# Kernel tuning notes

Hardware: AMD Instinct MI355X
Metric: run time of the kernel (lower is better)

## Reference

```python
import jax, jax.numpy as jnp
import numpy as np

B, T, N, C = 32, 12, 1024, 2   # batch, lookback window, n_series, in_channels
D, H, K, OUT = 16, 64, 2, 12   # embedding_dim, rnn_units, cheb_k, out_dim (horizon)


def setup_inputs() -> dict:
    key = jax.random.key(0)
    ks = jax.random.split(key, 12)
    p = lambda k, sh, s=0.1: jax.random.normal(k, sh, dtype=jnp.float32) * s
    return {
        "source": jax.random.normal(ks[0], (B, T, N, C), dtype=jnp.float32),
        "node_emb": p(ks[1], (N, D), 0.3),
        # layer 0: dim_in = C + H
        "gate_w0": p(ks[2], (D, K, C + H, 2 * H)),
        "gate_b0": p(ks[3], (D, 2 * H)),
        "upd_w0": p(ks[4], (D, K, C + H, H)),
        "upd_b0": p(ks[5], (D, H)),
        # layer 1: dim_in = H + H
        "gate_w1": p(ks[6], (D, K, 2 * H, 2 * H)),
        "gate_b1": p(ks[7], (D, 2 * H)),
        "upd_w1": p(ks[8], (D, K, 2 * H, H)),
        "upd_b1": p(ks[9], (D, H)),
        # end_conv: Conv2d(1, OUT*out_channels, kernel=(1,H)) == linear over hidden dim
        "conv_w": p(ks[10], (OUT, H)),
        "conv_b": p(ks[11], (OUT,)),
    }


def _supports(node_emb):
    # softmax(relu(E E^T)) row-normalized adaptive adjacency; Chebyshev stack (K, N, N)
    A = jax.nn.softmax(jax.nn.relu(node_emb @ node_emb.T), axis=1)
    s = [jnp.eye(N, dtype=A.dtype), A]
    for _ in range(2, K):
        s.append(2.0 * A @ s[-1] - s[-2])
    return jnp.stack(s, axis=0)


def _gcn(x, node_emb, w_pool, b_pool, supports):
    # x: (B, N, Cin); per-node adaptive weights from pools
    w = jnp.einsum('nd,dkio->nkio', node_emb, w_pool)     # (N, K, Cin, Cout)
    b = node_emb @ b_pool                                 # (N, Cout)
    xg = jnp.einsum('knm,bmc->bnkc', supports, x)         # (B, N, K, Cin)
    return jnp.einsum('bnki,nkio->bno', xg, w) + b


def _layer(x_seq, node_emb, supports, gw, gb, uw, ub):
    # x_seq: (B, T, N, Cin) -> (B, T, N, H) via GRU-style AGCRN cell, scanned over T
    def step(state, x_t):
        inp = jnp.concatenate([x_t, state], axis=-1)
        zr = jax.nn.sigmoid(_gcn(inp, node_emb, gw, gb, supports))
        z, r = jnp.split(zr, 2, axis=-1)
        cand = jnp.concatenate([x_t, z * state], axis=-1)
        hc = jnp.tanh(_gcn(cand, node_emb, uw, ub, supports))
        h = r * state + (1.0 - r) * hc
        return h, h

    init = jnp.zeros((x_seq.shape[0], N, H), dtype=x_seq.dtype)
    _, hs = jax.lax.scan(step, init, jnp.swapaxes(x_seq, 0, 1))
    return jnp.swapaxes(hs, 0, 1)


def reference(source, node_emb, gate_w0, gate_b0, upd_w0, upd_b0,
              gate_w1, gate_b1, upd_w1, upd_b1, conv_w, conv_b,
              teacher_forcing_ratio=0):
    sup = _supports(node_emb)  # adaptive supports depend only on static node_emb
    h1 = _layer(source, node_emb, sup, gate_w0, gate_b0, upd_w0, upd_b0)
    h2 = _layer(h1, node_emb, sup, gate_w1, gate_b1, upd_w1, upd_b1)
    last = h2[:, -1]  # (B, N, H)
    # end_conv over hidden dim -> (B, OUT, N); out_channels==1 so squeeze folds away
    out = jnp.einsum('bnh,oh->bon', last, conv_w) + conv_b[None, :, None]
    return out
```

## Files before the change

### kernel.cpp

```cpp
#include <hip/hip_runtime.h>
#include <hip/hip_fp16.h>


typedef _Float16 f16x8 __attribute__((ext_vector_type(8)));
typedef _Float16 f16x4 __attribute__((ext_vector_type(4)));
typedef float f32x4 __attribute__((ext_vector_type(4)));

#define WAIT_VM0 asm volatile("s_waitcnt vmcnt(0)" ::: "memory")
#define WAIT_VM1 asm volatile("s_waitcnt vmcnt(1)" ::: "memory")
#define WAIT_VM2 asm volatile("s_waitcnt vmcnt(2)" ::: "memory")
#define WAIT_VM1_LG asm volatile("s_waitcnt vmcnt(1) lgkmcnt(0)" ::: "memory")
#define WAIT_VM2_LG asm volatile("s_waitcnt vmcnt(2) lgkmcnt(0)" ::: "memory")
#define WAIT_LG asm volatile("s_waitcnt lgkmcnt(0)" ::: "memory")
#define BARRIER do { __builtin_amdgcn_s_barrier(); asm volatile("" ::: "memory"); } while (0)

__device__ __forceinline__ void gload_lds16(const void* g, void* l) {
  __builtin_amdgcn_global_load_lds(
      (const __attribute__((address_space(1))) void*)g,
      (__attribute__((address_space(3))) void*)l, 16, 0, 0);
}

__device__ __forceinline__ void dma_g128(const _Float16* Wc, _Float16* buf, int tid) {
  int wave = tid >> 6;
#pragma unroll
  for (int u = 0; u < 2; ++u) {
    gload_lds16(Wc + (size_t)(u * 256 + tid) * 8,
                buf + (size_t)(u * 256 + wave * 64) * 8);
  }
}

__device__ __forceinline__ void dma_g64(const _Float16* Wc, _Float16* buf, int tid) {
  int wave = tid >> 6;
  gload_lds16(Wc + (size_t)tid * 8, buf + (size_t)(wave * 64) * 8);
}

__device__ __forceinline__ f16x8 wrd(const _Float16* buf, int o, int s) {
  int flat = (o & 7) | (((s ^ (o & 3)) & 3) << 3) | ((o >> 3) << 5);
  return *(const f16x8*)(buf + flat * 8);
}

__global__ __launch_bounds__(256) void compute_A_kernel(const float* __restrict__ E,
                                                        __half* __restrict__ Ah) {
  int n = blockIdx.x;
  int tid = threadIdx.x;
  __shared__ float red[256];
  float en[16];
#pragma unroll
  for (int d = 0; d < 16; ++d) en[d] = E[n * 16 + d];
  float v[4];
#pragma unroll
  for (int q = 0; q < 4; ++q) {
    int m = tid + q * 256;
    const float* Em = E + m * 16;
    float dot = 0.f;
#pragma unroll
    for (int d = 0; d < 16; ++d) dot += en[d] * Em[d];
    v[q] = fmaxf(dot, 0.f);
  }
  float mx = fmaxf(fmaxf(v[0], v[1]), fmaxf(v[2], v[3]));
  red[tid] = mx; __syncthreads();
  for (int s = 128; s > 0; s >>= 1) { if (tid < s) red[tid] = fmaxf(red[tid], red[tid + s]); __syncthreads(); }
  mx = red[0];
  __syncthreads();
  float e[4], sum = 0.f;
#pragma unroll
  for (int q = 0; q < 4; ++q) { e[q] = expf(v[q] - mx); sum += e[q]; }
  red[tid] = sum; __syncthreads();
  for (int s = 128; s > 0; s >>= 1) { if (tid < s) red[tid] += red[tid + s]; __syncthreads(); }
  float inv = 1.f / red[0];
#pragma unroll
  for (int q = 0; q < 4; ++q) Ah[(size_t)n * 1024 + tid + q * 256] = __float2half(e[q] * inv);
}

__global__ __launch_bounds__(256) void pool_t16_kernel(const float* __restrict__ gw0,
                                                       const float* __restrict__ uw0,
                                                       const float* __restrict__ gw1,
                                                       const float* __restrict__ uw1,
                                                       __half* __restrict__ poolT16) {
  int rg = blockIdx.x;
  const float* pool; int F, O, TK; size_t jb; int kk, jj, i;
  if (rg < 128)      { pool = gw0; F = 66;  O = 128; TK = 64;  jb = 0;     kk = rg >> 6; jj = rg & 63; i = jj + 2; }
  else if (rg < 256) { int r = rg - 128; pool = uw0; F = 66;  O = 64;  TK = 64;  jb = 16384; kk = r >> 6; jj = r & 63;  i = jj + 2; }
  else if (rg < 512) { int r = rg - 256; pool = gw1; F = 128; O = 128; TK = 128; jb = 24576; kk = r >> 7; jj = r & 127; i = jj; }
  else               { int r = rg - 512; pool = uw1; F = 128; O = 64;  TK = 128; jb = 57344; kk = r >> 7; jj = r & 127; i = jj; }
  int o = threadIdx.x;
  if (o >= O) return;
  f16x8 a, b, zz = {};
#pragma unroll
  for (int d = 0; d < 8; ++d)
    a[d] = (_Float16)pool[(((size_t)d * 2 + kk) * F + i) * O + o];
#pragma unroll
  for (int d = 8; d < 16; ++d)
    b[d - 8] = (_Float16)pool[(((size_t)d * 2 + kk) * F + i) * O + o];
  size_t j = jb + (size_t)o * (2 * TK) + (size_t)kk * TK + jj;
  _Float16* outp = (_Float16*)poolT16 + j * 32;
  *(f16x8*)outp = a;
  *(f16x8*)(outp + 8) = b;
  *(f16x8*)(outp + 16) = zz;
  *(f16x8*)(outp + 24) = zz;
}

__global__ __launch_bounds__(256) void prelude_misc_kernel(
    const float* __restrict__ E, __half* __restrict__ E16,
    const float* __restrict__ gb0, const float* __restrict__ ub0,
    const float* __restrict__ gb1, const float* __restrict__ ub1,
    float* __restrict__ Bg0, float* __restrict__ Bu0,
    float* __restrict__ Bg1, float* __restrict__ Bu1,
    const float* __restrict__ src, __half* __restrict__ x16,
    const float* __restrict__ gw0, const float* __restrict__ uw0,
    float* __restrict__ WxG0, float* __restrict__ WxU0,
    float4* __restrict__ zero_p) {
  int bid = blockIdx.x;
  if (bid < 8192) {
    int i = bid * 256 + threadIdx.x;
    zero_p[i] = float4{0.f, 0.f, 0.f, 0.f};
    return;
  }
  bid -= 8192;
  if (bid < 384) {
    int t0 = bid >> 5, b = bid & 31;
    const float* s = src + (size_t)(b * 12 + t0) * 2048;
    __half* dst = x16 + t0 * 64 + b * 2;
    for (int nn = threadIdx.x; nn < 1024; nn += 256) {
      float2 v = *(const float2*)(s + nn * 2);
      *(__half2*)(dst + (size_t)nn * 768) = __floats2half2_rn(v.x, v.y);
    }
    return;
  }
  bid -= 384;
  if (bid < 1536) {
    int tid = bid * 256 + threadIdx.x;
    if (tid >= 1024 * 384) return;
    int n = tid / 384, c = tid - n * 384;
    const float* pool; float* outp; int O, o;
    if (c < 128)      { pool = gb0; outp = Bg0; O = 128; o = c; }
    else if (c < 192) { pool = ub0; outp = Bu0; O = 64;  o = c - 128; }
    else if (c < 320) { pool = gb1; outp = Bg1; O = 128; o = c - 192; }
    else              { pool = ub1; outp = Bu1; O = 64;  o = c - 320; }
    const float* En = E + n * 16;
    float a = 0.f;
#pragma unroll
    for (int d = 0; d < 16; ++d) a += En[d] * pool[d * O + o];
    outp[n * O + o] = a;
    return;
  }
  bid -= 1536;
  if (bid < 128) {
    int t = bid * 256 + threadIdx.x;
    int d = t & 31;
    E16[t] = (d < 16) ? __float2half(E[(t >> 5) * 16 + d]) : __half(0);
    return;
  }
  bid -= 128;
  if (bid < 2048) {
    int v = bid * 256 + threadIdx.x;
    int n = v >> 9, q = (v >> 7) & 3, o = v & 127;
    int kk = q >> 1, c = q & 1;
    const float* En = E + n * 16;
    float a = 0.f;
#pragma unroll
    for (int d = 0; d < 16; ++d)
      a += En[d] * gw0[(((size_t)d * 2 + kk) * 66 + c) * 128 + o];
    WxG0[(size_t)n * 512 + q * 128 + o] = __half2float(__float2half(a));
    return;
  }
  bid -= 2048;
  {
    int v = bid * 256 + threadIdx.x;
    int n = v >> 8, q = (v >> 6) & 3, o = v & 63;
    int kk = q >> 1, c = q & 1;
    const float* En = E + n * 16;
    float a = 0.f;
#pragma unroll
    for (int d = 0; d < 16; ++d)
      a += En[d] * uw0[(((size_t)d * 2 + kk) * 66 + c) * 64 + o];
    WxU0[(size_t)n * 256 + q * 64 + o] = __half2float(__float2half(a));
  }
}

__global__ __launch_bounds__(256) void make_wt_mfma_kernel(
    const __half* __restrict__ E16g, const __half* __restrict__ poolT16g,
    __half* __restrict__ WtG0, __half* __restrict__ WtU0,
    __half* __restrict__ WtG1, __half* __restrict__ WtU1) {
  __shared__ __align__(16) _Float16 Es[64][40];
  __shared__ __align__(16) _Float16 wbuf[64][264];
  const _Float16* E16 = (const _Float16*)E16g;
  const _Float16* pT = (const _Float16*)poolT16g;
  int bx = blockIdx.x;
  __half* Wt; int O, KIP, segbase, kc, og;
  if (bx < 64)       { Wt = WtG0; O = 128; KIP = 128; segbase = 0;     kc = bx & 3;  og = bx >> 2; }
  else if (bx < 96)  { int b = bx - 64;  Wt = WtU0; O = 64;  KIP = 128; segbase = 16384; kc = b & 3; og = b >> 2; }
  else if (bx < 224) { int b = bx - 96;  Wt = WtG1; O = 128; KIP = 256; segbase = 24576; kc = b & 7; og = b >> 3; }
  else               { int b = bx - 224; Wt = WtU1; O = 64;  KIP = 256; segbase = 57344; kc = b & 7; og = b >> 3; }
  int o0 = og * 8;
  int n0 = blockIdx.y * 64;
  {
    int r = threadIdx.x >> 2, ch = (threadIdx.x & 3) * 8;
    *(f16x8*)&Es[r][ch] = *(const f16x8*)(E16 + (size_t)(n0 + r) * 32 + ch);
  }
  __syncthreads();
  int wave = threadIdx.x >> 6, lane = threadIdx.x & 63;
  int fm = lane & 15, fg = lane >> 4;
  f16x8 af[4];
#pragma unroll
  for (int i = 0; i < 4; ++i) af[i] = *(const f16x8*)&Es[i * 16 + fm][fg * 8];
  f32x4 acc[4][4] = {};
#pragma unroll
  for (int jt = 0; jt < 4; ++jt) {
    int local = wave * 64 + jt * 16 + fm;
    int oo = local >> 5, kip = local & 31;
    size_t jc = (size_t)segbase + (size_t)(o0 + oo) * KIP + kc * 32 + kip;
    f16x8 bf = *(const f16x8*)(pT + jc * 32 + fg * 8);
#pragma unroll
    for (int i = 0; i < 4; ++i)
      acc[i][jt] = __builtin_amdgcn_mfma_f32_16x16x32_f16(af[i], bf, acc[i][jt], 0, 0, 0);
  }
#pragma unroll
  for (int i = 0; i < 4; ++i)
#pragma unroll
    for (int jt = 0; jt < 4; ++jt)
#pragma unroll
      for (int r = 0; r < 4; ++r)
        wbuf[i * 16 + fg * 4 + r][wave * 64 + jt * 16 + fm] = (_Float16)acc[i][jt][r];
  __syncthreads();
  int NCH = KIP >> 5;
  int CH = O * 32;
  int sbase = (o0 >> 3) * 256;
  for (int idx = threadIdx.x; idx < 64 * 32; idx += 256) {
    int nsub = idx >> 5, w = idx & 31;
    int oo = w & 7;
    int s = (w >> 3) ^ (w & 3);
    int pos = oo * 32 + s * 8;
    size_t dst = ((size_t)(n0 + nsub) * NCH + kc) * CH + sbase + (size_t)w * 8;
    *(float4*)(Wt + dst) = *(float4*)&wbuf[nsub][pos];
  }
}

__global__ __launch_bounds__(256) void gemm_nt_kernel(
    const __half* __restrict__ Ahg, const __half* __restrict__ X0g,
    const __half* __restrict__ X1g, __half* __restrict__ Yg,
    int Nc, int cstride, int split) {
  __shared__ __align__(16) _Float16 As[64][136];
  __shared__ __align__(16) _Float16 Bs[64][144];
  const _Float16* __restrict__ Ah = (const _Float16*)Ahg;
  _Float16* __restrict__ Y = (_Float16*)Yg;
  int tid = threadIdx.x;
  int row0 = blockIdx.y * 64;
  int col0 = blockIdx.x * 64;
  const _Float16* __restrict__ Xsrc =
      (col0 < split) ? (const _Float16*)X0g : (const _Float16*)X1g;
  int colg = (col0 < split) ? col0 : col0 - split;
  int wave = tid >> 6, lane = tid & 63;
  int wm = wave & 1, wn = wave >> 1;
  int fm = lane & 15, fg = lane >> 4;

  int sr = tid >> 2, sc = (tid & 3) * 32;
  const _Float16* pa = Ah + (size_t)(row0 + sr) * 1024 + sc;
  int kq = tid & 31, cg = tid >> 5;
  int kb = 4 * kq;
  const _Float16* pb = Xsrc + (size_t)kb * cstride + colg + cg * 8;
  int chunk = kq >> 1;
  int kin = (kq & 1) * 4;

  f16x8 ra[4], rb[4];
#pragma unroll
  for (int c = 0; c < 4; ++c) ra[c] = *(const f16x8*)(pa + c * 8);
#pragma unroll
  for (int r = 0; r < 4; ++r) rb[r] = *(const f16x8*)(pb + (size_t)r * cstride);

  f32x4 acc[2][2] = {};
  for (int k0 = 0; k0 < 1024; k0 += 128) {
#pragma unroll
    for (int c = 0; c < 4; ++c) *(f16x8*)&As[sr][sc + c * 8] = ra[c];
#pragma unroll
    for (int i = 0; i < 8; ++i) {
      int c = cg * 8 + i;
      f16x4 p;
      p[0] = rb[0][i]; p[1] = rb[1][i]; p[2] = rb[2][i]; p[3] = rb[3][i];
      *(f16x4*)&Bs[c][((chunk ^ (c & 7)) << 3) + kin] = p;
    }
    __syncthreads();
    if (k0 + 128 < 1024) {
#pragma unroll
      for (int c = 0; c < 4; ++c) ra[c] = *(const f16x8*)(pa + k0 + 128 + c * 8);
#pragma unroll
      for (int r = 0; r < 4; ++r)
        rb[r] = *(const f16x8*)(pb + (size_t)(k0 + 128 + r) * cstride);
    }
#pragma unroll
    for (int kc = 0; kc < 4; ++kc) {
      int ck = kc * 4 + fg;
      f16x8 af[2], bf[2];
#pragma unroll
      for (int i = 0; i < 2; ++i)
        af[i] = *(const f16x8*)&As[wm * 32 + i * 16 + fm][kc * 32 + fg * 8];
#pragma unroll
      for (int j = 0; j < 2; ++j) {
        int cl = wn * 32 + j * 16 + fm;
        bf[j] = *(const f16x8*)&Bs[cl][(ck ^ (cl & 7)) << 3];
      }
#pragma unroll
      for (int i = 0; i < 2; ++i)
#pragma unroll
        for (int j = 0; j < 2; ++j)
          acc[i][j] = __builtin_amdgcn_mfma_f32_16x16x32_f16(af[i], bf[j], acc[i][j], 0, 0, 0);
    }
    __syncthreads();
  }
#pragma unroll
  for (int i = 0; i < 2; ++i) {
#pragma unroll
    for (int j = 0; j < 2; ++j) {
      int col = col0 + wn * 32 + j * 16 + fm;
      int rbase = row0 + wm * 32 + i * 16 + fg * 4;
#pragma unroll
      for (int r = 0; r < 4; ++r)
        Y[(size_t)(rbase + r) * Nc + col] = (_Float16)acc[i][j][r];
    }
  }
}

__global__ __launch_bounds__(256) void gemm_nt128_kernel(
    const __half* __restrict__ Ahg, const __half* __restrict__ X0g,
    const __half* __restrict__ X1g, __half* __restrict__ Yg,
    int Nc, int cstride, int split) {
  __shared__ __align__(16) _Float16 As[64][136];
  __shared__ __align__(16) _Float16 Bs[128][144];
  const _Float16* __restrict__ Ah = (const _Float16*)Ahg;
  _Float16* __restrict__ Y = (_Float16*)Yg;
  int tid = threadIdx.x;
  int row0 = blockIdx.y * 64;
  int col0 = blockIdx.x * 128;
  const _Float16* __restrict__ Xsrc =
      (col0 < split) ? (const _Float16*)X0g : (const _Float16*)X1g;
  int colg = (col0 < split) ? col0 : col0 - split;
  int wave = tid >> 6, lane = tid & 63;
  int fm = lane & 15, fg = lane >> 4;

  int sr = tid >> 2, sc = (tid & 3) * 32;
  const _Float16* pa = Ah + (size_t)(row0 + sr) * 1024 + sc;
  int kq = tid & 31, cg = tid >> 5;
  int kb = 4 * kq;
  const _Float16* pb = Xsrc + (size_t)kb * cstride + colg + cg * 16;
  int chunk = kq >> 1;
  int kin = (kq & 1) * 4;

  f16x8 ra[4], rb[4][2];
#pragma unroll
  for (int c = 0; c < 4; ++c) ra[c] = *(const f16x8*)(pa + c * 8);
#pragma unroll
  for (int r = 0; r < 4; ++r)
#pragma unroll
    for (int h = 0; h < 2; ++h)
      rb[r][h] = *(const f16x8*)(pb + (size_t)r * cstride + h * 8);

  f32x4 acc[4][2] = {};
  for (int k0 = 0; k0 < 1024; k0 += 128) {
#pragma unroll
    for (int c = 0; c < 4; ++c) *(f16x8*)&As[sr][sc + c * 8] = ra[c];
#pragma unroll
    for (int h = 0; h < 2; ++h)
#pragma unroll
      for (int i = 0; i < 8; ++i) {
        int c = cg * 16 + h * 8 + i;
        f16x4 p;
        p[0] = rb[0][h][i]; p[1] = rb[1][h][i]; p[2] = rb[2][h][i]; p[3] = rb[3][h][i];
        *(f16x4*)&Bs[c][((chunk ^ (c & 7)) << 3) + kin] = p;
      }
    __syncthreads();
    if (k0 + 128 < 1024) {
#pragma unroll
      for (int c = 0; c < 4; ++c) ra[c] = *(const f16x8*)(pa + k0 + 128 + c * 8);
#pragma unroll
      for (int r = 0; r < 4; ++r)
#pragma unroll
        for (int h = 0; h < 2; ++h)
          rb[r][h] = *(const f16x8*)(pb + (size_t)(k0 + 128 + r) * cstride + h * 8);
    }
#pragma unroll
    for (int kc = 0; kc < 4; ++kc) {
      int ck = kc * 4 + fg;
      f16x8 af[4], bf[2];
#pragma unroll
      for (int i = 0; i < 4; ++i)
        af[i] = *(const f16x8*)&As[i * 16 + fm][kc * 32 + fg * 8];
#pragma unroll
      for (int j = 0; j < 2; ++j) {
        int cl = wave * 32 + j * 16 + fm;
        bf[j] = *(const f16x8*)&Bs[cl][(ck ^ (cl & 7)) << 3];
      }
#pragma unroll
      for (int i = 0; i < 4; ++i)
#pragma unroll
        for (int j = 0; j < 2; ++j)
          acc[i][j] = __builtin_amdgcn_mfma_f32_16x16x32_f16(af[i], bf[j], acc[i][j], 0, 0, 0);
    }
    __syncthreads();
  }
#pragma unroll
  for (int i = 0; i < 4; ++i) {
#pragma unroll
    for (int j = 0; j < 2; ++j) {
      int col = col0 + wave * 32 + j * 16 + fm;
      int rbase = row0 + i * 16 + fg * 4;
#pragma unroll
      for (int r = 0; r < 4; ++r)
        Y[(size_t)(rbase + r) * Nc + col] = (_Float16)acc[i][j][r];
    }
  }
}

__device__ __forceinline__ f16x8 ld_g0(const __half* __restrict__ h16,
                                       const __half* __restrict__ YBD, int n, int idx) {
  int b = idx >> 4, part = (idx >> 3) & 1, ch = idx & 7;
  const _Float16* s = part ? (const _Float16*)YBD + (size_t)n * 4096 + b * 64 + ch * 8
                           : (const _Float16*)h16 + (size_t)n * 2048 + b * 64 + ch * 8;
  return *(const f16x8*)s;
}
__device__ __forceinline__ f16x8 ld_u0(const __half* __restrict__ zh0,
                                       const __half* __restrict__ YCE, int n, int idx) {
  int b = idx >> 4, part = (idx >> 3) & 1, ch = idx & 7;
  const _Float16* s = part ? (const _Float16*)YCE + (size_t)n * 4096 + 2048 + b * 64 + ch * 8
                           : (const _Float16*)zh0 + (size_t)n * 2048 + b * 64 + ch * 8;
  return *(const f16x8*)s;
}

__device__ __forceinline__ void gate0_body(
    _Float16* Xs, float (*xq)[4], _Float16 (*Wb)[4096], int n, int t,
    f16x8 pre0, f16x8 pre1, float2 xv, unsigned axu,
    const _Float16* Wn, const float* __restrict__ Bg, const float* __restrict__ Wxg,
    const float* __restrict__ h32, __half* __restrict__ zh0, __half* __restrict__ r0) {
  constexpr int STRIDE = 136;
  {
    int b0 = t >> 4, p0 = (t >> 3) & 1, c0 = t & 7;
    *(f16x8*)&Xs[b0 * STRIDE + p0 * 64 + c0 * 8] = pre0;
    int idx = t + 256;
    int b1 = idx >> 4, p1 = (idx >> 3) & 1, c1 = idx & 7;
    *(f16x8*)&Xs[b1 * STRIDE + p1 * 64 + c1 * 8] = pre1;
  }
  if (t < 32) {
    __half2 ah = *(__half2*)&axu;
    float2 af2 = __half22float2(ah);
    xq[t][0] = __half2float(__float2half(xv.x));
    xq[t][1] = __half2float(__float2half(xv.y));
    xq[t][2] = af2.x; xq[t][3] = af2.y;
  }
  int wave = t >> 6, lane = t & 63;
  int fm = lane & 15, fg = lane >> 4;
  f32x4 acc[2][2] = {};
#pragma unroll
  for (int kc = 0; kc < 4; ++kc) {
    if (kc == 0) WAIT_VM2_LG;
    else if (kc < 3) WAIT_VM2;
    else WAIT_VM0;
    BARRIER;
    const _Float16* wb = Wb[kc & 1];
    f16x8 af[2], bf[2];
#pragma unroll
    for (int i = 0; i < 2; ++i)
      af[i] = *(const f16x8*)&Xs[(i * 16 + fm) * STRIDE + kc * 32 + fg * 8];
#pragma unroll
    for (int j = 0; j < 2; ++j)
      bf[j] = wrd(wb, wave * 32 + j * 16 + fm, fg);
    WAIT_LG;
    BARRIER;
    if (kc < 2) dma_g128(Wn + (size_t)(kc + 2) * 4096, Wb[kc & 1], t);
    __builtin_amdgcn_s_setprio(1);
#pragma unroll
    for (int i = 0; i < 2; ++i)
#pragma unroll
      for (int j = 0; j < 2; ++j)
        acc[i][j] = __builtin_amdgcn_mfma_f32_16x16x32_f16(af[i], bf[j], acc[i][j], 0, 0, 0);
    __builtin_amdgcn_s_setprio(0);
  }
  const float* Bn = Bg + n * 128;
  const float* Wx = Wxg + (size_t)n * 512;
#pragma unroll
  for (int j = 0; j < 2; ++j) {
    int o = wave * 32 + j * 16 + fm;
    float bias = Bn[o];
    float w0 = Wx[o], w1 = Wx[128 + o], w2 = Wx[256 + o], w3 = Wx[384 + o];
#pragma unroll
    for (int i = 0; i < 2; ++i)
#pragma unroll
      for (int r = 0; r < 4; ++r) {
        int b = i * 16 + fg * 4 + r;
        float px = acc[i][j][r] + bias +
                   w0 * xq[b][0] + w1 * xq[b][1] + w2 * xq[b][2] + w3 * xq[b][3];
        float s = 1.f / (1.f + __expf(-px));
        size_t base = (size_t)n * 2048 + b * 64;
        if (o < 64) zh0[base + o] = __float2half(s * h32[base + o]);
        else        r0[base + o - 64] = __float2half(s);
      }
  }
}

__device__ __forceinline__ void upd0_body(
    _Float16* Xs, float (*xq)[4], _Float16 (*Wb)[2048], int n, int t,
    f16x8 pre0, f16x8 pre1, float2 xv, unsigned axu,
    const _Float16* Wn, const float* __restrict__ Bu, const float* __restrict__ Wxu,
    const __half* __restrict__ r0, float* __restrict__ h32, __half* __restrict__ h16) {
  constexpr int STRIDE = 136;
  {
    int b0 = t >> 4, p0 = (t >> 3) & 1, c0 = t & 7;
    *(f16x8*)&Xs[b0 * STRIDE + p0 * 64 + c0 * 8] = pre0;
    int idx = t + 256;
    int b1 = idx >> 4, p1 = (idx >> 3) & 1, c1 = idx & 7;
    *(f16x8*)&Xs[b1 * STRIDE + p1 * 64 + c1 * 8] = pre1;
  }
  if (t < 32) {
    __half2 ah = *(__half2*)&axu;
    float2 af2 = __half22float2(ah);
    xq[t][0] = __half2float(__float2half(xv.x));
    xq[t][1] = __half2float(__float2half(xv.y));
    xq[t][2] = af2.x; xq[t][3] = af2.y;
  }
  int wave = t >> 6, lane = t & 63;
  int fm = lane & 15, fg = lane >> 4;
  f32x4 acc[2] = {};
#pragma unroll
  for (int kc = 0; kc < 4; ++kc) {
    if (kc == 0) WAIT_VM1_LG;
    else if (kc < 3) WAIT_VM1;
    else WAIT_VM0;
    BARRIER;
    const _Float16* wb = Wb[kc & 1];
    f16x8 bf = wrd(wb, wave * 16 + fm, fg);
    f16x8 af0 = *(const f16x8*)&Xs[(0 * 16 + fm) * STRIDE + kc * 32 + fg * 8];
    f16x8 af1 = *(const f16x8*)&Xs[(1 * 16 + fm) * STRIDE + kc * 32 + fg * 8];
    WAIT_LG;
    BARRIER;
    if (kc < 2) dma_g64(Wn + (size_t)(kc + 2) * 2048, Wb[kc & 1], t);
    __builtin_amdgcn_s_setprio(1);
    acc[0] = __builtin_amdgcn_mfma_f32_16x16x32_f16(af0, bf, acc[0], 0, 0, 0);
    acc[1] = __builtin_amdgcn_mfma_f32_16x16x32_f16(af1, bf, acc[1], 0, 0, 0);
    __builtin_amdgcn_s_setprio(0);
  }
  int o = wave * 16 + fm;
  float bias = Bu[n * 64 + o];
  const float* Wx = Wxu + (size_t)n * 256;
  float w0 = Wx[o], w1 = Wx[64 + o], w2 = Wx[128 + o], w3 = Wx[192 + o];
#pragma unroll
  for (int i = 0; i < 2; ++i)
#pragma unroll
    for (int r = 0; r < 4; ++r) {
      int b = i * 16 + fg * 4 + r;
      float x = acc[i][r] + bias +
                w0 * xq[b][0] + w1 * xq[b][1] + w2 * xq[b][2] + w3 * xq[b][3];
      x = fminf(fmaxf(x, -15.f), 15.f);
      float e = __expf(2.f * x);
      float hc = (e - 1.f) / (e + 1.f);
      size_t base = (size_t)n * 2048 + b * 64;
      float rr = __half2float(r0[base + o]);
      float hnew = rr * h32[base + o] + (1.f - rr) * hc;
      h32[base + o] = hnew;
      h16[base + o] = __float2half(hnew);
    }
}

__global__ __launch_bounds__(256) void gate0_kernel(
    const __half* __restrict__ h16, const __half* __restrict__ YBD,
    const float* __restrict__ src, const __half* __restrict__ Axt, int tstep,
    const __half* __restrict__ Wtg, const float* __restrict__ Bg,
    const float* __restrict__ Wxg,
    const float* __restrict__ h32, __half* __restrict__ zh0, __half* __restrict__ r0) {
  __shared__ __align__(16) _Float16 Xs[32 * 136];
  __shared__ __align__(16) _Float16 Wb[2][4096];
  __shared__ float xq[32][4];
  int n = blockIdx.x, t = threadIdx.x;
  const _Float16* Wn = (const _Float16*)Wtg + (size_t)n * 16384;
  f16x8 p0 = ld_g0(h16, YBD, n, t);
  f16x8 p1 = ld_g0(h16, YBD, n, t + 256);
  float2 xv = {}; unsigned ax = 0;
  if (t < 32) {
    xv = *(const float2*)(src + ((size_t)(t * 12 + tstep) * 1024 + n) * 2);
    ax = *(const unsigned*)((const _Float16*)Axt + (size_t)n * 768 + tstep * 64 + t * 2);
  }
  dma_g128(Wn, Wb[0], t);
  dma_g128(Wn + 4096, Wb[1], t);
  gate0_body(Xs, xq, Wb, n, t, p0, p1, xv, ax, Wn, Bg, Wxg, h32, zh0, r0);
}

__global__ __launch_bounds__(256) void upd0_kernel(
    const __half* __restrict__ zh0, const __half* __restrict__ YCE,
    const float* __restrict__ src, const __half* __restrict__ Axt, int tstep,
    const __half* __restrict__ Wtg, const float* __restrict__ Bu,
    const float* __restrict__ Wxu,
    const __half* __restrict__ r0, float* __restrict__ h32, __half* __restrict__ h16) {
  __shared__ __align__(16) _Float16 Xs[32 * 136];
  __shared__ __align__(16) _Float16 Wb[2][2048];
  __shared__ float xq[32][4];
  int n = blockIdx.x, t = threadIdx.x;
  const _Float16* Wn = (const _Float16*)Wtg + (size_t)n * 8192;
  f16x8 p0 = ld_u0(zh0, YCE, n, t);
  f16x8 p1 = ld_u0(zh0, YCE, n, t + 256);
  float2 xv = {}; unsigned ax = 0;
  if (t < 32) {
    xv = *(const float2*)(src + ((size_t)(t * 12 + tstep) * 1024 + n) * 2);
    ax = *(const unsigned*)((const _Float16*)Axt + (size_t)n * 768 + tstep * 64 + t * 2);
  }
  dma_g64(Wn, Wb[0], t);
  dma_g64(Wn + 2048, Wb[1], t);
  upd0_body(Xs, xq, Wb, n, t, p0, p1, xv, ax, Wn, Bu, Wxu, r0, h32, h16);
}

__global__ __launch_bounds__(256) void gate1_gate0_kernel(
    const __half* __restrict__ h1_16, const __half* __restrict__ h2_16,
    const __half* __restrict__ YBD,
    const __half* __restrict__ WtG1, const float* __restrict__ Bg1,
    const float* __restrict__ h2_32, __half* __restrict__ zh1, __half* __restrict__ r1,
    const float* __restrict__ src, const __half* __restrict__ Axt, int tnext,
    const __half* __restrict__ WtG0, const float* __restrict__ Bg0,
    const float* __restrict__ WxG0,
    const float* __restrict__ h1_32, __half* __restrict__ zh0, __half* __restrict__ r0,
    int do_gate0) {
  constexpr int STRIDE = 264;
  __shared__ __align__(16) _Float16 Xs[32 * STRIDE];
  __shared__ __align__(16) _Float16 Wb[2][4096];
  __shared__ float xq[32][4];
  int n = blockIdx.x;
  int t = threadIdx.x;
  const _Float16* Wn1 = (const _Float16*)WtG1 + (size_t)n * 32768;
  const _Float16* Wn0 = (const _Float16*)WtG0 + (size_t)n * 16384;
  f16x8 s1[4];
#pragma unroll
  for (int u = 0; u < 4; ++u) {
    int idx = t + u * 256;
    int b = idx >> 5, q = idx & 31;
    const _Float16* s;
    if (q < 8)       s = (const _Float16*)h1_16 + (size_t)n * 2048 + b * 64 + q * 8;
    else if (q < 16) s = (const _Float16*)h2_16 + (size_t)n * 2048 + b * 64 + (q - 8) * 8;
    else if (q < 24) s = (const _Float16*)YBD + (size_t)n * 4096 + b * 64 + (q - 16) * 8;
    else             s = (const _Float16*)YBD + (size_t)n * 4096 + 2048 + b * 64 + (q - 24) * 8;
    s1[u] = *(const f16x8*)s;
  }
  f16x8 g0p0 = {}, g0p1 = {}; float2 g0xv = {}; unsigned g0ax = 0;
  if (do_gate0) {
    g0p0 = ld_g0(h1_16, YBD, n, t);
    g0p1 = ld_g0(h1_16, YBD, n, t + 256);
    if (t < 32) {
      g0xv = *(const float2*)(src + ((size_t)(t * 12 + tnext) * 1024 + n) * 2);
      g0ax = *(const unsigned*)((const _Float16*)Axt + (size_t)n * 768 + tnext * 64 + t * 2);
    }
  }
  dma_g128(Wn1, Wb[0], t);
  dma_g128(Wn1 + 4096, Wb[1], t);
#pragma unroll
  for (int u = 0; u < 4; ++u) {
    int idx = t + u * 256;
    int b = idx >> 5, q = idx & 31;
    *(f16x8*)&Xs[b * STRIDE + q * 8] = s1[u];
  }
  int wave = t >> 6, lane = t & 63;
  int fm = lane & 15, fg = lane >> 4;
  {
    f32x4 acc[2][2] = {};
#pragma unroll
    for (int kc = 0; kc < 8; ++kc) {
      if (kc == 0) WAIT_VM2_LG;
      else if (kc < 7) WAIT_VM2;
      else { if (do_gate0) WAIT_VM2; else WAIT_VM0; }
      BARRIER;
      const _Float16* wb = Wb[kc & 1];
      f16x8 af[2], bf[2];
#pragma unroll
      for (int i = 0; i < 2; ++i)
        af[i] = *(const f16x8*)&Xs[(i * 16 + fm) * STRIDE + kc * 32 + fg * 8];
#pragma unroll
      for (int j = 0; j < 2; ++j)
        bf[j] = wrd(wb, wave * 32 + j * 16 + fm, fg);
      WAIT_LG;
      BARRIER;
      if (kc < 6) dma_g128(Wn1 + (size_t)(kc + 2) * 4096, Wb[kc & 1], t);
      else if (do_gate0) dma_g128(Wn0 + (size_t)(kc - 6) * 4096, Wb[kc & 1], t);
      __builtin_amdgcn_s_setprio(1);
#pragma unroll
      for (int i = 0; i < 2; ++i)
#pragma unroll
        for (int j = 0; j < 2; ++j)
          acc[i][j] = __builtin_amdgcn_mfma_f32_16x16x32_f16(af[i], bf[j], acc[i][j], 0, 0, 0);
      __builtin_amdgcn_s_setprio(0);
    }
    const float* Bn = Bg1 + n * 128;
#pragma unroll
    for (int j = 0; j < 2; ++j) {
      int o = wave * 32 + j * 16 + fm;
      float bias = Bn[o];
#pragma unroll
      for (int i = 0; i < 2; ++i)
#pragma unroll
        for (int r = 0; r < 4; ++r) {
          int b = i * 16 + fg * 4 + r;
          float s = 1.f / (1.f + __expf(-(acc[i][j][r] + bias)));
          size_t base = (size_t)n * 2048 + b * 64;
          if (o < 64) zh1[base + o] = __float2half(s * h2_32[base + o]);
          else        r1[base + o - 64] = __float2half(s);
        }
    }
  }
  if (!do_gate0) return;
  gate0_body(Xs, xq, Wb, n, t, g0p0, g0p1, g0xv, g0ax, Wn0, Bg0, WxG0, h1_32, zh0, r0);
}

__global__ __launch_bounds__(256) void upd1_upd0_kernel(
    const __half* __restrict__ h1_16, const __half* __restrict__ zh1,
    const __half* __restrict__ YBD, const __half* __restrict__ YCE,
    const __half* __restrict__ WtU1, const float* __restrict__ Bu1,
    const __half* __restrict__ r1, float* __restrict__ h2_32, __half* __restrict__ h2_16,
    const __half* __restrict__ zh0,
    const float* __restrict__ src, const __half* __restrict__ Axt, int tnext,
    const __half* __restrict__ WtU0, const float* __restrict__ Bu0,
    const float* __restrict__ WxU0,
    const __half* __restrict__ r0, float* __restrict__ h1_32, __half* __restrict__ h1_16w,
    int do_upd0) {
  constexpr int STRIDE = 264;
  __shared__ __align__(16) _Float16 Xs[32 * STRIDE];
  __shared__ __align__(16) _Float16 Wb[2][2048];
  __shared__ float xq[32][4];
  int n = blockIdx.x;
  int t = threadIdx.x;
  const _Float16* Wn1 = (const _Float16*)WtU1 + (size_t)n * 16384;
  const _Float16* Wn0 = (const _Float16*)WtU0 + (size_t)n * 8192;
  f16x8 s1[4];
#pragma unroll
  for (int u = 0; u < 4; ++u) {
    int idx = t + u * 256;
    int b = idx >> 5, q = idx & 31;
    const _Float16* s;
    if (q < 8)       s = (const _Float16*)h1_16 + (size_t)n * 2048 + b * 64 + q * 8;
    else if (q < 16) s = (const _Float16*)zh1 + (size_t)n * 2048 + b * 64 + (q - 8) * 8;
    else if (q < 24) s = (const _Float16*)YBD + (size_t)n * 4096 + b * 64 + (q - 16) * 8;
    else             s = (const _Float16*)YCE + (size_t)n * 4096 + b * 64 + (q - 24) * 8;
    s1[u] = *(const f16x8*)s;
  }
  f16x8 u0p0 = {}, u0p1 = {}; float2 u0xv = {}; unsigned u0ax = 0;
  if (do_upd0) {
    u0p0 = ld_u0(zh0, YCE, n, t);
    u0p1 = ld_u0(zh0, YCE, n, t + 256);
    if (t < 32) {
      u0xv = *(const float2*)(src + ((size_t)(t * 12 + tnext) * 1024 + n) * 2);
      u0ax = *(const unsigned*)((const _Float16*)Axt + (size_t)n * 768 + tnext * 64 + t * 2);
    }
  }
  dma_g64(Wn1, Wb[0], t);
  dma_g64(Wn1 + 2048, Wb[1], t);
#pragma unroll
  for (int u = 0; u < 4; ++u) {
    int idx = t + u * 256;
    int b = idx >> 5, q = idx & 31;
    *(f16x8*)&Xs[b * STRIDE + q * 8] = s1[u];
  }
  int wave = t >> 6, lane = t & 63;
  int fm = lane & 15, fg = lane >> 4;
  {
    f32x4 acc[2] = {};
#pragma unroll
    for (int kc = 0; kc < 8; ++kc) {
      if (kc == 0) WAIT_VM1_LG;
      else if (kc < 7) WAIT_VM1;
      else { if (do_upd0) WAIT_VM1; else WAIT_VM0; }
      BARRIER;
      const _Float16* wb = Wb[kc & 1];
      f16x8 bf = wrd(wb, wave * 16 + fm, fg);
      f16x8 af0 = *(const f16x8*)&Xs[(0 * 16 + fm) * STRIDE + kc * 32 + fg * 8];
      f16x8 af1 = *(const f16x8*)&Xs[(1 * 16 + fm) * STRIDE + kc * 32 + fg * 8];
      WAIT_LG;
      BARRIER;
      if (kc < 6) dma_g64(Wn1 + (size_t)(kc + 2) * 2048, Wb[kc & 1], t);
      else if (do_upd0) dma_g64(Wn0 + (size_t)(kc - 6) * 2048, Wb[kc & 1], t);
      __builtin_amdgcn_s_setprio(1);
      acc[0] = __builtin_amdgcn_mfma_f32_16x16x32_f16(af0, bf, acc[0], 0, 0, 0);
      acc[1] = __builtin_amdgcn_mfma_f32_16x16x32_f16(af1, bf, acc[1], 0, 0, 0);
      __builtin_amdgcn_s_setprio(0);
    }
    int o = wave * 16 + fm;
    float bias = Bu1[n * 64 + o];
#pragma unroll
    for (int i = 0; i < 2; ++i)
#pragma unroll
      for (int r = 0; r < 4; ++r) {
        int b = i * 16 + fg * 4 + r;
        float x = acc[i][r] + bias;
        x = fminf(fmaxf(x, -15.f), 15.f);
        float e = __expf(2.f * x);
        float hc = (e - 1.f) / (e + 1.f);
        size_t base = (size_t)n * 2048 + b * 64;
        float rr = __half2float(r1[base + o]);
        float hnew = rr * h2_32[base + o] + (1.f - rr) * hc;
        h2_32[base + o] = hnew;
        h2_16[base + o] = __float2half(hnew);
      }
  }
  if (!do_upd0) return;
  upd0_body(Xs, xq, Wb, n, t, u0p0, u0p1, u0xv, u0ax, Wn0, Bu0, WxU0, r0, h1_32, h1_16w);
}

__global__ void final_conv_kernel(const float* __restrict__ h2, const float* __restrict__ cw,
                                  const float* __restrict__ cb, float* __restrict__ out) {
  int tid = blockIdx.x * 256 + threadIdx.x;
  if (tid >= 32 * 1024) return;
  int n = tid & 1023, b = tid >> 10;
  const float* hp = h2 + ((size_t)n * 32 + b) * 64;
  float hv[64];
#pragma unroll
  for (int i = 0; i < 64; ++i) hv[i] = hp[i];
#pragma unroll
  for (int o = 0; o < 12; ++o) {
    float acc = cb[o];
#pragma unroll
    for (int i = 0; i < 64; ++i) acc += hv[i] * cw[o * 64 + i];
    out[((size_t)b * 12 + o) * 1024 + n] = acc;
  }
}

extern "C" void kernel_launch(void* const* d_in, const int* in_sizes, int n_in,
                              void* d_out, int out_size, void* d_ws, size_t ws_size,
                              hipStream_t stream) {
  const float* src = (const float*)d_in[0];
  const float* E   = (const float*)d_in[1];
  const float* gw0 = (const float*)d_in[2];
  const float* gb0 = (const float*)d_in[3];
  const float* uw0 = (const float*)d_in[4];
  const float* ub0 = (const float*)d_in[5];
  const float* gw1 = (const float*)d_in[6];
  const float* gb1 = (const float*)d_in[7];
  const float* uw1 = (const float*)d_in[8];
  const float* ub1 = (const float*)d_in[9];
  const float* cw  = (const float*)d_in[10];
  const float* cb  = (const float*)d_in[11];
  float* out = (float*)d_out;
  (void)in_sizes; (void)n_in; (void)out_size; (void)ws_size;

  char* base = (char*)d_ws;
  size_t off = 0;
  auto alloc = [&](size_t bytes) -> void* {
    void* p = base + off; off += (bytes + 511) & ~(size_t)511; return p;
  };
  __half* Ah   = (__half*)alloc((size_t)1024 * 1024 * 2);
  __half* WtG0 = (__half*)alloc((size_t)1024 * 128 * 128 * 2);
  __half* WtU0 = (__half*)alloc((size_t)1024 * 64 * 128 * 2);
  __half* WtG1 = (__half*)alloc((size_t)1024 * 128 * 256 * 2);
  __half* WtU1 = (__half*)alloc((size_t)1024 * 64 * 256 * 2);
  float*  Bg0  = (float*) alloc((size_t)1024 * 128 * 4);
  float*  Bu0  = (float*) alloc((size_t)1024 * 64 * 4);
  float*  Bg1  = (float*) alloc((size_t)1024 * 128 * 4);
  float*  Bu1  = (float*) alloc((size_t)1024 * 64 * 4);
  float*  WxG0 = (float*) alloc((size_t)1024 * 512 * 4);
  float*  WxU0 = (float*) alloc((size_t)1024 * 256 * 4);
  float*  h1_32 = (float*)alloc((size_t)1024 * 2048 * 4);
  float*  h2_32 = (float*)alloc((size_t)1024 * 2048 * 4);
  __half* h1_16 = (__half*)alloc((size_t)1024 * 2048 * 2);
  __half* h2_16 = (__half*)alloc((size_t)1024 * 2048 * 2);
  __half* YBD  = (__half*)alloc((size_t)1024 * 4096 * 2);
  __half* YCE  = (__half*)alloc((size_t)1024 * 4096 * 2);
  __half* zh0  = (__half*)alloc((size_t)1024 * 2048 * 2);
  __half* zh1  = (__half*)alloc((size_t)1024 * 2048 * 2);
  __half* Axt  = (__half*)alloc((size_t)1024 * 768 * 2);
  __half* r1   = (__half*)alloc((size_t)1024 * 2048 * 2);
  __half* r0   = (__half*)alloc((size_t)1024 * 2048 * 2);
  __half* poolT16 = (__half*)alloc((size_t)73728 * 32 * 2);
  __half* E16  = (__half*)alloc((size_t)1024 * 32 * 2);
  __half* x16  = (__half*)alloc((size_t)1024 * 768 * 2);

  compute_A_kernel<<<1024, 256, 0, stream>>>(E, Ah);
  prelude_misc_kernel<<<13312, 256, 0, stream>>>(E, E16, gb0, ub0, gb1, ub1,
                                                 Bg0, Bu0, Bg1, Bu1,
                                                 src, x16, gw0, uw0, WxG0, WxU0,
                                                 (float4*)h1_32);
  pool_t16_kernel<<<768, 256, 0, stream>>>(gw0, uw0, gw1, uw1, poolT16);
  make_wt_mfma_kernel<<<dim3(288, 16), 256, 0, stream>>>(E16, poolT16, WtG0, WtU0, WtG1, WtU1);
  gemm_nt_kernel<<<dim3(12, 16), 256, 0, stream>>>(Ah, (__half*)x16, (__half*)x16, Axt,
                                                   768, 768, 768);

  gate0_kernel<<<1024, 256, 0, stream>>>(h1_16, YBD, src, Axt, 0, WtG0, Bg0, WxG0,
                                         h1_32, zh0, r0);
  gemm_nt128_kernel<<<dim3(16, 16), 256, 0, stream>>>(Ah, zh0, zh0, YCE + 2048,
                                                      4096, 2048, 2048);
  upd0_kernel<<<1024, 256, 0, stream>>>(zh0, YCE, src, Axt, 0, WtU0, Bu0, WxU0,
                                        r0, h1_32, h1_16);

  for (int t = 0; t < 12; ++t) {
    int more = (t < 11) ? 1 : 0;
    gemm_nt128_kernel<<<dim3(32, 16), 256, 0, stream>>>(Ah, h1_16, h2_16, YBD,
                                                        4096, 2048, 2048);
    gate1_gate0_kernel<<<1024, 256, 0, stream>>>(h1_16, h2_16, YBD, WtG1, Bg1, h2_32, zh1, r1,
                                                 src, Axt, t + 1, WtG0, Bg0, WxG0,
                                                 h1_32, zh0, r0, more);
    gemm_nt128_kernel<<<dim3(32, 16), 256, 0, stream>>>(Ah, zh1, zh0, YCE,
                                                        4096, 2048, 2048);
    upd1_upd0_kernel<<<1024, 256, 0, stream>>>(h1_16, zh1, YBD, YCE, WtU1, Bu1, r1,
                                               h2_32, h2_16, zh0, src, Axt, t + 1,
                                               WtU0, Bu0, WxU0, r0, h1_32, h1_16, more);
  }

  final_conv_kernel<<<(32 * 1024 + 255) / 256, 256, 0, stream>>>(h2_32, cw, cb, out);
}
```

Baseline: 1.324 ms.

## Store gate weights as FP8 and dequantize to FP16 in LDS reads

The per-node gate weight tensors for both layers are now written in FP8 (E4M3/E5M2 via cvt_pk_fp8) instead of FP16, which halves the bytes streamed from HBM per gate chunk. The DMA helper now issues one 16-byte load per thread per 4KB chunk, and the wait counts are adjusted to match. The weights are converted back to FP16 in registers before the MFMA. This cuts weight bandwidth in the memory-bound recurrent gate kernels, at the cost of extra conversion ALU work and reduced weight precision, which may affect accuracy tolerance.

New measurement: 1.242 ms, median of 2. -6.2%, faster.

```diff
diff --git a/kernel.cpp b/kernel.cpp
--- a/kernel.cpp
+++ b/kernel.cpp
@@ -5,12 +5,11 @@
 typedef _Float16 f16x8 __attribute__((ext_vector_type(8)));
 typedef _Float16 f16x4 __attribute__((ext_vector_type(4)));
 typedef float f32x4 __attribute__((ext_vector_type(4)));
+typedef float f32x2 __attribute__((ext_vector_type(2)));
 
 #define WAIT_VM0 asm volatile("s_waitcnt vmcnt(0)" ::: "memory")
 #define WAIT_VM1 asm volatile("s_waitcnt vmcnt(1)" ::: "memory")
-#define WAIT_VM2 asm volatile("s_waitcnt vmcnt(2)" ::: "memory")
 #define WAIT_VM1_LG asm volatile("s_waitcnt vmcnt(1) lgkmcnt(0)" ::: "memory")
-#define WAIT_VM2_LG asm volatile("s_waitcnt vmcnt(2) lgkmcnt(0)" ::: "memory")
 #define WAIT_LG asm volatile("s_waitcnt lgkmcnt(0)" ::: "memory")
 #define BARRIER do { __builtin_amdgcn_s_barrier(); asm volatile("" ::: "memory"); } while (0)
 
@@ -20,13 +19,8 @@
       (__attribute__((address_space(3))) void*)l, 16, 0, 0);
 }
 
-__device__ __forceinline__ void dma_g128(const _Float16* Wc, _Float16* buf, int tid) {
-  int wave = tid >> 6;
-#pragma unroll
-  for (int u = 0; u < 2; ++u) {
-    gload_lds16(Wc + (size_t)(u * 256 + tid) * 8,
-                buf + (size_t)(u * 256 + wave * 64) * 8);
-  }
+__device__ __forceinline__ void dma_b4k(const unsigned char* Wc, unsigned char* buf, int tid) {
+  gload_lds16(Wc + (size_t)tid * 16, buf + (size_t)tid * 16);
 }
 
 __device__ __forceinline__ void dma_g64(const _Float16* Wc, _Float16* buf, int tid) {
@@ -37,6 +31,22 @@
 __device__ __forceinline__ f16x8 wrd(const _Float16* buf, int o, int s) {
   int flat = (o & 7) | (((s ^ (o & 3)) & 3) << 3) | ((o >> 3) << 5);
   return *(const f16x8*)(buf + flat * 8);
+}
+
+__device__ __forceinline__ f16x8 wrd8(const unsigned char* buf, int o, int s) {
+  int flat = (o & 7) | (((s ^ (o & 3)) & 3) << 3) | ((o >> 3) << 5);
+  const unsigned* p = (const unsigned*)(buf + flat * 8);
+  unsigned lo = p[0], hi = p[1];
+  f32x2 a0 = __builtin_amdgcn_cvt_pk_f32_fp8(lo, 0);
+  f32x2 a1 = __builtin_amdgcn_cvt_pk_f32_fp8(lo, 1);
+  f32x2 a2 = __builtin_amdgcn_cvt_pk_f32_fp8(hi, 0);
+  f32x2 a3 = __builtin_amdgcn_cvt_pk_f32_fp8(hi, 1);
+  f16x8 r;
+  r[0] = (_Float16)a0[0]; r[1] = (_Float16)a0[1];
+  r[2] = (_Float16)a1[0]; r[3] = (_Float16)a1[1];
+  r[4] = (_Float16)a2[0]; r[5] = (_Float16)a2[1];
+  r[6] = (_Float16)a3[0]; r[7] = (_Float16)a3[1];
+  return r;
 }
 
 __global__ __launch_bounds__(256) void compute_A_kernel(const float* __restrict__ E,
@@ -180,18 +190,18 @@
 
 __global__ __launch_bounds__(256) void make_wt_mfma_kernel(
     const __half* __restrict__ E16g, const __half* __restrict__ poolT16g,
-    __half* __restrict__ WtG0, __half* __restrict__ WtU0,
-    __half* __restrict__ WtG1, __half* __restrict__ WtU1) {
+    unsigned char* __restrict__ WtG0, __half* __restrict__ WtU0,
+    unsigned char* __restrict__ WtG1, __half* __restrict__ WtU1) {
   __shared__ __align__(16) _Float16 Es[64][40];
   __shared__ __align__(16) _Float16 wbuf[64][264];
   const _Float16* E16 = (const _Float16*)E16g;
   const _Float16* pT = (const _Float16*)poolT16g;
   int bx = blockIdx.x;
-  __half* Wt; int O, KIP, segbase, kc, og;
-  if (bx < 64)       { Wt = WtG0; O = 128; KIP = 128; segbase = 0;     kc = bx & 3;  og = bx >> 2; }
-  else if (bx < 96)  { int b = bx - 64;  Wt = WtU0; O = 64;  KIP = 128; segbase = 16384; kc = b & 3; og = b >> 2; }
-  else if (bx < 224) { int b = bx - 96;  Wt = WtG1; O = 128; KIP = 256; segbase = 24576; kc = b & 7; og = b >> 3; }
-  else               { int b = bx - 224; Wt = WtU1; O = 64;  KIP = 256; segbase = 57344; kc = b & 7; og = b >> 3; }
+  void* Wt; int O, KIP, segbase, kc, og, fp8;
+  if (bx < 64)       { Wt = WtG0; O = 128; KIP = 128; segbase = 0;     kc = bx & 3;  og = bx >> 2; fp8 = 1; }
+  else if (bx < 96)  { int b = bx - 64;  Wt = WtU0; O = 64;  KIP = 128; segbase = 16384; kc = b & 3; og = b >> 2; fp8 = 0; }
+  else if (bx < 224) { int b = bx - 96;  Wt = WtG1; O = 128; KIP = 256; segbase = 24576; kc = b & 7; og = b >> 3; fp8 = 1; }
+  else               { int b = bx - 224; Wt = WtU1; O = 64;  KIP = 256; segbase = 57344; kc = b & 7; og = b >> 3; fp8 = 0; }
   int o0 = og * 8;
   int n0 = blockIdx.y * 64;
   {
@@ -224,15 +234,34 @@
         wbuf[i * 16 + fg * 4 + r][wave * 64 + jt * 16 + fm] = (_Float16)acc[i][jt][r];
   __syncthreads();
   int NCH = KIP >> 5;
-  int CH = O * 32;
-  int sbase = (o0 >> 3) * 256;
-  for (int idx = threadIdx.x; idx < 64 * 32; idx += 256) {
-    int nsub = idx >> 5, w = idx & 31;
-    int oo = w & 7;
-    int s = (w >> 3) ^ (w & 3);
-    int pos = oo * 32 + s * 8;
-    size_t dst = ((size_t)(n0 + nsub) * NCH + kc) * CH + sbase + (size_t)w * 8;
-    *(float4*)(Wt + dst) = *(float4*)&wbuf[nsub][pos];
+  if (fp8) {
+    int CHB = O * 32;
+    int sbaseB = (o0 >> 3) * 256;
+    for (int idx = threadIdx.x; idx < 64 * 32; idx += 256) {
+      int nsub = idx >> 5, w = idx & 31;
+      int oo = w & 7;
+      int s = (w >> 3) ^ (w & 3);
+      int pos = oo * 32 + s * 8;
+      const _Float16* v = &wbuf[nsub][pos];
+      unsigned d0 = __builtin_amdgcn_cvt_pk_fp8_f32((float)v[0], (float)v[1], 0, 0);
+      d0 = __builtin_amdgcn_cvt_pk_fp8_f32((float)v[2], (float)v[3], d0, 1);
+      unsigned d1 = __builtin_amdgcn_cvt_pk_fp8_f32((float)v[4], (float)v[5], 0, 0);
+      d1 = __builtin_amdgcn_cvt_pk_fp8_f32((float)v[6], (float)v[7], d1, 1);
+      size_t dst = ((size_t)(n0 + nsub) * NCH + kc) * CHB + sbaseB + (size_t)w * 8;
+      uint2 u; u.x = d0; u.y = d1;
+      *(uint2*)((unsigned char*)Wt + dst) = u;
+    }
+  } else {
+    int CH = O * 32;
+    int sbase = (o0 >> 3) * 256;
+    for (int idx = threadIdx.x; idx < 64 * 32; idx += 256) {
+      int nsub = idx >> 5, w = idx & 31;
+      int oo = w & 7;
+      int s = (w >> 3) ^ (w & 3);
+      int pos = oo * 32 + s * 8;
+      size_t dst = ((size_t)(n0 + nsub) * NCH + kc) * CH + sbase + (size_t)w * 8;
+      *(float4*)((__half*)Wt + dst) = *(float4*)&wbuf[nsub][pos];
+    }
   }
 }
 
@@ -426,9 +455,9 @@
 }
 
 __device__ __forceinline__ void gate0_body(
-    _Float16* Xs, float (*xq)[4], _Float16 (*Wb)[4096], int n, int t,
+    _Float16* Xs, float (*xq)[4], unsigned char (*Wb)[4096], int n, int t,
     f16x8 pre0, f16x8 pre1, float2 xv, unsigned axu,
-    const _Float16* Wn, const float* __restrict__ Bg, const float* __restrict__ Wxg,
+    const unsigned char* Wn, const float* __restrict__ Bg, const float* __restrict__ Wxg,
     const float* __restrict__ h32, __half* __restrict__ zh0, __half* __restrict__ r0) {
   constexpr int STRIDE = 136;
   {
@@ -450,21 +479,21 @@
   f32x4 acc[2][2] = {};
 #pragma unroll
   for (int kc = 0; kc < 4; ++kc) {
-    if (kc == 0) WAIT_VM2_LG;
-    else if (kc < 3) WAIT_VM2;
+    if (kc == 0) WAIT_VM1_LG;
+    else if (kc < 3) WAIT_VM1;
     else WAIT_VM0;
     BARRIER;
-    const _Float16* wb = Wb[kc & 1];
+    const unsigned char* wb = Wb[kc & 1];
     f16x8 af[2], bf[2];
 #pragma unroll
     for (int i = 0; i < 2; ++i)
       af[i] = *(const f16x8*)&Xs[(i * 16 + fm) * STRIDE + kc * 32 + fg * 8];
 #pragma unroll
     for (int j = 0; j < 2; ++j)
-      bf[j] = wrd(wb, wave * 32 + j * 16 + fm, fg);
+      bf[j] = wrd8(wb, wave * 32 + j * 16 + fm, fg);
     WAIT_LG;
     BARRIER;
-    if (kc < 2) dma_g128(Wn + (size_t)(kc + 2) * 4096, Wb[kc & 1], t);
+    if (kc < 2) dma_b4k(Wn + (size_t)(kc + 2) * 4096, Wb[kc & 1], t);
     __builtin_amdgcn_s_setprio(1);
 #pragma unroll
     for (int i = 0; i < 2; ++i)
@@ -561,14 +590,14 @@
 __global__ __launch_bounds__(256) void gate0_kernel(
     const __half* __restrict__ h16, const __half* __restrict__ YBD,
     const float* __restrict__ src, const __half* __restrict__ Axt, int tstep,
-    const __half* __restrict__ Wtg, const float* __restrict__ Bg,
+    const unsigned char* __restrict__ Wtg, const float* __restrict__ Bg,
     const float* __restrict__ Wxg,
     const float* __restrict__ h32, __half* __restrict__ zh0, __half* __restrict__ r0) {
   __shared__ __align__(16) _Float16 Xs[32 * 136];
-  __shared__ __align__(16) _Float16 Wb[2][4096];
+  __shared__ __align__(16) unsigned char Wb[2][4096];
   __shared__ float xq[32][4];
   int n = blockIdx.x, t = threadIdx.x;
-  const _Float16* Wn = (const _Float16*)Wtg + (size_t)n * 16384;
+  const unsigned char* Wn = Wtg + (size_t)n * 16384;
   f16x8 p0 = ld_g0(h16, YBD, n, t);
   f16x8 p1 = ld_g0(h16, YBD, n, t + 256);
   float2 xv = {}; unsigned ax = 0;
@@ -576,8 +605,8 @@
     xv = *(const float2*)(src + ((size_t)(t * 12 + tstep) * 1024 + n) * 2);
     ax = *(const unsigned*)((const _Float16*)Axt + (size_t)n * 768 + tstep * 64 + t * 2);
   }
-  dma_g128(Wn, Wb[0], t);
-  dma_g128(Wn + 4096, Wb[1], t);
+  dma_b4k(Wn, Wb[0], t);
+  dma_b4k(Wn + 4096, Wb[1], t);
   gate0_body(Xs, xq, Wb, n, t, p0, p1, xv, ax, Wn, Bg, Wxg, h32, zh0, r0);
 }
 
@@ -607,21 +636,21 @@
 __global__ __launch_bounds__(256) void gate1_gate0_kernel(
     const __half* __restrict__ h1_16, const __half* __restrict__ h2_16,
     const __half* __restrict__ YBD,
-    const __half* __restrict__ WtG1, const float* __restrict__ Bg1,
+    const unsigned char* __restrict__ WtG1, const float* __restrict__ Bg1,
     const float* __restrict__ h2_32, __half* __restrict__ zh1, __half* __restrict__ r1,
     const float* __restrict__ src, const __half* __restrict__ Axt, int tnext,
-    const __half* __restrict__ WtG0, const float* __restrict__ Bg0,
+    const unsigned char* __restrict__ WtG0, const float* __restrict__ Bg0,
     const float* __restrict__ WxG0,
     const float* __restrict__ h1_32, __half* __restrict__ zh0, __half* __restrict__ r0,
     int do_gate0) {
   constexpr int STRIDE = 264;
   __shared__ __align__(16) _Float16 Xs[32 * STRIDE];
-  __shared__ __align__(16) _Float16 Wb[2][4096];
+  __shared__ __align__(16) unsigned char Wb[2][4096];
   __shared__ float xq[32][4];
   int n = blockIdx.x;
   int t = threadIdx.x;
-  const _Float16* Wn1 = (const _Float16*)WtG1 + (size_t)n * 32768;
-  const _Float16* Wn0 = (const _Float16*)WtG0 + (size_t)n * 16384;
+  const unsigned char* Wn1 = WtG1 + (size_t)n * 32768;
+  const unsigned char* Wn0 = WtG0 + (size_t)n * 16384;
   f16x8 s1[4];
 #pragma unroll
   for (int u = 0; u < 4; ++u) {
@@ -643,8 +672,8 @@
       g0ax = *(const unsigned*)((const _Float16*)Axt + (size_t)n * 768 + tnext * 64 + t * 2);
     }
   }
-  dma_g128(Wn1, Wb[0], t);
-  dma_g128(Wn1 + 4096, Wb[1], t);
+  dma_b4k(Wn1, Wb[0], t);
+  dma_b4k(Wn1 + 4096, Wb[1], t);
 #pragma unroll
   for (int u = 0; u < 4; ++u) {
     int idx = t + u * 256;
@@ -657,22 +686,22 @@
     f32x4 acc[2][2] = {};
 #pragma unroll
     for (int kc = 0; kc < 8; ++kc) {
-      if (kc == 0) WAIT_VM2_LG;
-      else if (kc < 7) WAIT_VM2;
-      else { if (do_gate0) WAIT_VM2; else WAIT_VM0; }
+      if (kc == 0) WAIT_VM1_LG;
+      else if (kc < 7) WAIT_VM1;
+      else { if (do_gate0) WAIT_VM1; else WAIT_VM0; }
       BARRIER;
-      const _Float16* wb = Wb[kc & 1];
+      const unsigned char* wb = Wb[kc & 1];
       f16x8 af[2], bf[2];
 #pragma unroll
       for (int i = 0; i < 2; ++i)
         af[i] = *(const f16x8*)&Xs[(i * 16 + fm) * STRIDE + kc * 32 + fg * 8];
 #pragma unroll
       for (int j = 0; j < 2; ++j)
-        bf[j] = wrd(wb, wave * 32 + j * 16 + fm, fg);
+        bf[j] = wrd8(wb, wave * 32 + j * 16 + fm, fg);
       WAIT_LG;
       BARRIER;
-      if (kc < 6) dma_g128(Wn1 + (size_t)(kc + 2) * 4096, Wb[kc & 1], t);
-      else if (do_gate0) dma_g128(Wn0 + (size_t)(kc - 6) * 4096, Wb[kc & 1], t);
+      if (kc < 6) dma_b4k(Wn1 + (size_t)(kc + 2) * 4096, Wb[kc & 1], t);
+      else if (do_gate0) dma_b4k(Wn0 + (size_t)(kc - 6) * 4096, Wb[kc & 1], t);
       __builtin_amdgcn_s_setprio(1);
 #pragma unroll
       for (int i = 0; i < 2; ++i)
@@ -837,9 +866,9 @@
     void* p = base + off; off += (bytes + 511) & ~(size_t)511; return p;
   };
   __half* Ah   = (__half*)alloc((size_t)1024 * 1024 * 2);
-  __half* WtG0 = (__half*)alloc((size_t)1024 * 128 * 128 * 2);
+  unsigned char* WtG0 = (unsigned char*)alloc((size_t)1024 * 16384);
   __half* WtU0 = (__half*)alloc((size_t)1024 * 64 * 128 * 2);
-  __half* WtG1 = (__half*)alloc((size_t)1024 * 128 * 256 * 2);
+  unsigned char* WtG1 = (unsigned char*)alloc((size_t)1024 * 32768);
   __half* WtU1 = (__half*)alloc((size_t)1024 * 64 * 256 * 2);
   float*  Bg0  = (float*) alloc((size_t)1024 * 128 * 4);
   float*  Bu0  = (float*) alloc((size_t)1024 * 64 * 4);
```
